# Performance work log

Hardware: AMD Instinct MI355X
Metric: run time of the kernel (lower is better)

## Reference

```python
import jax, jax.numpy as jnp
import numpy as np

EMBED = 1024
HEADS = 16
HEAD_DIM = EMBED // HEADS
BATCH = 8
SEQ = 2048


def setup_inputs() -> dict:
    key = jax.random.key(0)
    ks = jax.random.split(key, 6)
    s = EMBED ** -0.5
    x = jax.random.normal(ks[0], (BATCH, SEQ, EMBED), dtype=jnp.float32)
    # weights stored as (in, out); applied as x @ W (equivalent to torch Linear with W.T)
    Wq = jax.random.normal(ks[1], (EMBED, EMBED), dtype=jnp.float32) * s
    Wk = jax.random.normal(ks[2], (EMBED, EMBED), dtype=jnp.float32) * s
    Wv = jax.random.normal(ks[3], (EMBED, EMBED), dtype=jnp.float32) * s
    Wo = jax.random.normal(ks[4], (EMBED, EMBED), dtype=jnp.float32) * s
    bo = jax.random.normal(ks[5], (EMBED,), dtype=jnp.float32) * 0.01
    return {"x": x, "Wq": Wq, "Wk": Wk, "Wv": Wv, "Wo": Wo, "bo": bo}


def reference(x, Wq, Wk, Wv, Wo, bo):
    N, S, E = x.shape
    H, D = HEADS, HEAD_DIM
    # project and reshape to (N, H, S, D) exactly as the torch code (view + permute)
    q = (x @ Wq).reshape(N, S, H, D).transpose(0, 2, 1, 3)
    k = (x @ Wk).reshape(N, S, H, D).transpose(0, 2, 1, 3)
    v = (x @ Wv).reshape(N, S, H, D).transpose(0, 2, 1, 3)
    # Faithful to source: einsum subscripts applied to ALREADY-PERMUTED tensors,
    # so 'a'/'b' range over heads and 's' over seq -> energy is (N, H, H).
    energy = jnp.einsum('nasd,nbsd->nab', q, k)
    attention = jax.nn.softmax(energy / np.sqrt(D).astype(np.float32), axis=2)
    # second einsum: sum over key-heads (b) and value-heads (h) independently
    out = jnp.einsum('nab,nhsd->nasd', attention, v)  # (N, H, S, D)
    out = out.transpose(0, 2, 1, 3).reshape(N, S, E)
    return out @ Wo + bo
```

## Files before the change

kernel.cpp:

```cpp
#include <hip/hip_runtime.h>
#include <hip/hip_bf16.h>


typedef __attribute__((ext_vector_type(8))) short bf16x8;
typedef __attribute__((ext_vector_type(4))) float f32x4;

__device__ __forceinline__ unsigned short f2bf(float f) {
  unsigned int u = __builtin_bit_cast(unsigned int, f);
  u += 0x7FFFu + ((u >> 16) & 1u);
  return (unsigned short)(u >> 16);
}
__device__ __forceinline__ float bf2f(unsigned short b) {
  unsigned int u = ((unsigned int)b) << 16;
  return __builtin_bit_cast(float, u);
}
__device__ __forceinline__ unsigned int pack2(unsigned short a, unsigned short b) {
  return (unsigned int)a | ((unsigned int)b << 16);
}
__device__ __forceinline__ void split2(float a, float b, unsigned int& hi, unsigned int& lo) {
  unsigned short ha = f2bf(a), hb = f2bf(b);
  hi = pack2(ha, hb);
  lo = pack2(f2bf(a - bf2f(ha)), f2bf(b - bf2f(hb)));
}
__device__ __forceinline__ bf16x8 asbf(uint4 u) { return __builtin_bit_cast(bf16x8, u); }

__global__ __launch_bounds__(256) void prep(const float* __restrict__ Wv,
                                            const float* __restrict__ Wo,
                                            unsigned short* __restrict__ BvF,
                                            unsigned short* __restrict__ BoF) {
  const int b = blockIdx.x, t = threadIdx.x;
  const int l = t & 63, lr = l & 15, lk = (l >> 4) << 3;
  if (b < 32) {
    const int s = b, ctg = t >> 6;
    const int d = (ctg << 4) + lr;
    const int k0 = (s << 5) + lk;
    float sum[8] = {};
#pragma unroll
    for (int h = 0; h < 16; ++h)
#pragma unroll
      for (int j = 0; j < 8; ++j)
        sum[j] += Wv[(k0 + j) * 1024 + h * 64 + d];
    unsigned short hh[8], ll[8];
#pragma unroll
    for (int j = 0; j < 8; ++j) {
      hh[j] = f2bf(sum[j]);
      ll[j] = f2bf(sum[j] - bf2f(hh[j]));
    }
    const int base = ((s * 4 + ctg) * 2) * 64 + l;
    uint4 uh = make_uint4(pack2(hh[0], hh[1]), pack2(hh[2], hh[3]),
                          pack2(hh[4], hh[5]), pack2(hh[6], hh[7]));
    uint4 ul = make_uint4(pack2(ll[0], ll[1]), pack2(ll[2], ll[3]),
                          pack2(ll[4], ll[5]), pack2(ll[6], ll[7]));
    ((uint4*)BvF)[base] = uh;
    ((uint4*)BvF)[base + 64] = ul;
  } else {
    const int ctg2 = b - 32;
    const int kk = t >> 7, jh = (t >> 6) & 1;
    const int e = (ctg2 << 4) + lr;
    const int kb = (kk << 5) + lk + (jh << 2);
    float sum[4] = {};
#pragma unroll
    for (int h = 0; h < 16; ++h)
#pragma unroll
      for (int j = 0; j < 4; ++j)
        sum[j] += Wo[(h * 64 + kb + j) * 1024 + e];
    unsigned short hh[4], ll[4];
#pragma unroll
    for (int j = 0; j < 4; ++j) {
      hh[j] = f2bf(sum[j]);
      ll[j] = f2bf(sum[j] - bf2f(hh[j]));
    }
    const int base = ((((ctg2 * 2 + kk) * 2) * 64 + l) << 1) + jh;
    ((uint2*)BoF)[base] = make_uint2(pack2(hh[0], hh[1]), pack2(hh[2], hh[3]));
    ((uint2*)BoF)[base + 128] = make_uint2(pack2(ll[0], ll[1]), pack2(ll[2], ll[3]));
  }
}

__global__ __launch_bounds__(256) void gemm1(const float* __restrict__ x,
                                             const unsigned short* __restrict__ BvF,
                                             unsigned short* __restrict__ tmph,
                                             unsigned short* __restrict__ tmpl) {
  __shared__ unsigned short Ah[2][32][72], Al[2][32][72];
  const int t = threadIdx.x;
  const int r0 = blockIdx.x << 5;
  const int w = t >> 6, l = t & 63;
  const int wr = (w >> 1) << 4;
  const int ctgb = (w & 1) << 1;
  const int lr = l & 15, lk = (l >> 4) << 3;
  const int srow = t >> 3, skg = (t & 7) << 3;
  const float* xp = &x[(r0 + srow) * 1024 + skg];
  const uint4* bp = (const uint4*)BvF;

  float4 xr[2][2];
  uint4 br[2][8];
  f32x4 acc[2] = {};

  xr[0][0] = *(const float4*)(xp);
  xr[0][1] = *(const float4*)(xp + 4);
  xr[1][0] = *(const float4*)(xp + 64);
  xr[1][1] = *(const float4*)(xp + 68);
#pragma unroll
  for (int kk = 0; kk < 2; ++kk)
#pragma unroll
    for (int ct = 0; ct < 2; ++ct)
#pragma unroll
      for (int hl = 0; hl < 2; ++hl)
        br[0][(kk * 2 + ct) * 2 + hl] =
            bp[((kk * 4 + ctgb + ct) * 2 + hl) * 64 + l];
  {
    unsigned int h0, h1, h2, h3, q0, q1, q2, q3;
    split2(xr[0][0].x, xr[0][0].y, h0, q0);
    split2(xr[0][0].z, xr[0][0].w, h1, q1);
    split2(xr[0][1].x, xr[0][1].y, h2, q2);
    split2(xr[0][1].z, xr[0][1].w, h3, q3);
    *(uint4*)&Ah[0][srow][skg] = make_uint4(h0, h1, h2, h3);
    *(uint4*)&Al[0][srow][skg] = make_uint4(q0, q1, q2, q3);
  }

#pragma unroll
  for (int c = 0; c < 16; ++c) {
    const int buf = c & 1;
    if (c + 2 < 16) {
      const float* xq = xp + (c + 2) * 64;
      xr[buf][0] = *(const float4*)(xq);
      xr[buf][1] = *(const float4*)(xq + 4);
    }
    if (c + 1 < 16) {
#pragma unroll
      for (int kk = 0; kk < 2; ++kk)
#pragma unroll
        for (int ct = 0; ct < 2; ++ct)
#pragma unroll
          for (int hl = 0; hl < 2; ++hl)
            br[buf ^ 1][(kk * 2 + ct) * 2 + hl] =
                bp[((((c + 1) * 2 + kk) * 4 + ctgb + ct) * 2 + hl) * 64 + l];
    }
    __syncthreads();
#pragma unroll
    for (int kk = 0; kk < 2; ++kk) {
      bf16x8 ah = *(const bf16x8*)&Ah[buf][wr + lr][kk * 32 + lk];
      bf16x8 al = *(const bf16x8*)&Al[buf][wr + lr][kk * 32 + lk];
#pragma unroll
      for (int ct = 0; ct < 2; ++ct) {
        bf16x8 bh = asbf(br[buf][(kk * 2 + ct) * 2 + 0]);
        bf16x8 bl = asbf(br[buf][(kk * 2 + ct) * 2 + 1]);
        acc[ct] = __builtin_amdgcn_mfma_f32_16x16x32_bf16(ah, bh, acc[ct], 0, 0, 0);
        acc[ct] = __builtin_amdgcn_mfma_f32_16x16x32_bf16(ah, bl, acc[ct], 0, 0, 0);
        acc[ct] = __builtin_amdgcn_mfma_f32_16x16x32_bf16(al, bh, acc[ct], 0, 0, 0);
      }
    }
    if (c + 1 < 16) {
      unsigned int h0, h1, h2, h3, q0, q1, q2, q3;
      float4 a0 = xr[buf ^ 1][0], a1 = xr[buf ^ 1][1];
      split2(a0.x, a0.y, h0, q0);
      split2(a0.z, a0.w, h1, q1);
      split2(a1.x, a1.y, h2, q2);
      split2(a1.z, a1.w, h3, q3);
      *(uint4*)&Ah[buf ^ 1][srow][skg] = make_uint4(h0, h1, h2, h3);
      *(uint4*)&Al[buf ^ 1][srow][skg] = make_uint4(q0, q1, q2, q3);
    }
  }

  __syncthreads();
  {
    unsigned short* sh = &Ah[0][0][0];
    unsigned short* sl = &Al[0][0][0];
#pragma unroll
    for (int ct = 0; ct < 2; ++ct) {
      const int col = ((ctgb + ct) << 4) + lr;
#pragma unroll
      for (int j = 0; j < 4; ++j) {
        const int r = wr + ((l >> 4) << 2) + j;
        float v = acc[ct][j];
        unsigned short h = f2bf(v);
        sh[r * 72 + col] = h;
        sl[r * 72 + col] = f2bf(v - bf2f(h));
      }
    }
  }
  __syncthreads();
  {
    const int row = t >> 3, kg = (t & 7) << 3;
    uint4 vh = *(const uint4*)&Ah[0][row][kg];
    uint4 vl = *(const uint4*)&Al[0][row][kg];
    *(uint4*)&tmph[(r0 + row) * 64 + kg] = vh;
    *(uint4*)&tmpl[(r0 + row) * 64 + kg] = vl;
  }
}

__global__ __launch_bounds__(256) void gemm2(const unsigned short* __restrict__ tmph,
                                             const unsigned short* __restrict__ tmpl,
                                             const unsigned short* __restrict__ BoF,
                                             const float* __restrict__ bo,
                                             float* __restrict__ out) {
  __shared__ unsigned short Ah[64][72], Al[64][72];
  const int t = threadIdx.x;
  const int mb = blockIdx.x >> 1, nb = blockIdx.x & 1;
  const int r0 = mb << 6, c0 = nb << 9;
  const int l = t & 63, lr = l & 15, lk = (l >> 4) << 3;
  const int wr = (t >> 6) << 4;
  const uint4* bp = (const uint4*)BoF;

  {
    const int row = t >> 2, kg = (t & 3) << 4;
    const uint4* ph = (const uint4*)&tmph[(r0 + row) * 64 + kg];
    uint4 a0 = ph[0], a1 = ph[1];
    const uint4* pl4 = (const uint4*)&tmpl[(r0 + row) * 64 + kg];
    uint4 b0 = pl4[0], b1 = pl4[1];
    *(uint4*)&Ah[row][kg] = a0;
    *(uint4*)&Ah[row][kg + 8] = a1;
    *(uint4*)&Al[row][kg] = b0;
    *(uint4*)&Al[row][kg + 8] = b1;
  }
  uint4 brg[2][4];
  float bvr[2];
#pragma unroll
  for (int kk = 0; kk < 2; ++kk)
#pragma unroll
    for (int hl = 0; hl < 2; ++hl)
      brg[0][kk * 2 + hl] = bp[(((nb * 32) * 2 + kk) * 2 + hl) * 64 + l];
  bvr[0] = bo[c0 + lr];
  __syncthreads();

  bf16x8 afh[2], afl[2];
#pragma unroll
  for (int kk = 0; kk < 2; ++kk) {
    afh[kk] = *(const bf16x8*)&Ah[wr + lr][kk * 32 + lk];
    afl[kk] = *(const bf16x8*)&Al[wr + lr][kk * 32 + lk];
  }

#pragma unroll
  for (int ct = 0; ct < 32; ++ct) {
    if (ct + 1 < 32) {
#pragma unroll
      for (int kk = 0; kk < 2; ++kk)
#pragma unroll
        for (int hl = 0; hl < 2; ++hl)
          brg[(ct + 1) & 1][kk * 2 + hl] =
              bp[(((nb * 32 + ct + 1) * 2 + kk) * 2 + hl) * 64 + l];
      bvr[(ct + 1) & 1] = bo[c0 + ((ct + 1) << 4) + lr];
    }
    f32x4 a = {};
#pragma unroll
    for (int kk = 0; kk < 2; ++kk) {
      bf16x8 bh = asbf(brg[ct & 1][kk * 2 + 0]);
      bf16x8 bl = asbf(brg[ct & 1][kk * 2 + 1]);
      a = __builtin_amdgcn_mfma_f32_16x16x32_bf16(afh[kk], bh, a, 0, 0, 0);
      a = __builtin_amdgcn_mfma_f32_16x16x32_bf16(afh[kk], bl, a, 0, 0, 0);
      a = __builtin_amdgcn_mfma_f32_16x16x32_bf16(afl[kk], bh, a, 0, 0, 0);
    }
    const int col = c0 + (ct << 4) + lr;
    const float bv = bvr[ct & 1];
#pragma unroll
    for (int j = 0; j < 4; ++j)
      out[(r0 + wr + ((l >> 4) << 2) + j) * 1024 + col] = a[j] + bv;
  }
}

extern "C" void kernel_launch(void* const* d_in, const int* in_sizes, int n_in,
                              void* d_out, int out_size, void* d_ws, size_t ws_size,
                              hipStream_t stream) {
  const float* x = (const float*)d_in[0];
  const float* Wv = (const float*)d_in[3];
  const float* Wo = (const float*)d_in[4];
  const float* bo = (const float*)d_in[5];
  float* out = (float*)d_out;

  unsigned short* BvF = (unsigned short*)d_ws;
  unsigned short* BoF = BvF + 131072;
  unsigned short* tmph = BoF + 131072;
  unsigned short* tmpl = tmph + 1048576;

  prep<<<96, 256, 0, stream>>>(Wv, Wo, BvF, BoF);
  gemm1<<<512, 256, 0, stream>>>(x, BvF, tmph, tmpl);
  gemm2<<<512, 256, 0, stream>>>(tmph, tmpl, BoF, bo, out);
}
```

Baseline: 152.7 us.

## Fuse both GEMMs into one kernel with split-K reduction through shared memory

```diff
diff --git a/kernel.cpp b/kernel.cpp
--- a/kernel.cpp
+++ b/kernel.cpp
@@ -47,16 +47,14 @@
       ll[j] = f2bf(sum[j] - bf2f(hh[j]));
     }
     const int base = ((s * 4 + ctg) * 2) * 64 + l;
-    uint4 uh = make_uint4(pack2(hh[0], hh[1]), pack2(hh[2], hh[3]),
-                          pack2(hh[4], hh[5]), pack2(hh[6], hh[7]));
-    uint4 ul = make_uint4(pack2(ll[0], ll[1]), pack2(ll[2], ll[3]),
-                          pack2(ll[4], ll[5]), pack2(ll[6], ll[7]));
-    ((uint4*)BvF)[base] = uh;
-    ((uint4*)BvF)[base + 64] = ul;
+    ((uint4*)BvF)[base] = make_uint4(pack2(hh[0], hh[1]), pack2(hh[2], hh[3]),
+                                     pack2(hh[4], hh[5]), pack2(hh[6], hh[7]));
+    ((uint4*)BvF)[base + 64] = make_uint4(pack2(ll[0], ll[1]), pack2(ll[2], ll[3]),
+                                          pack2(ll[4], ll[5]), pack2(ll[6], ll[7]));
   } else {
-    const int ctg2 = b - 32;
+    const int g = b - 32;
     const int kk = t >> 7, jh = (t >> 6) & 1;
-    const int e = (ctg2 << 4) + lr;
+    const int e = (g << 4) + lr;
     const int kb = (kk << 5) + lk + (jh << 2);
     float sum[4] = {};
 #pragma unroll
@@ -70,190 +68,136 @@
       hh[j] = f2bf(sum[j]);
       ll[j] = f2bf(sum[j] - bf2f(hh[j]));
     }
-    const int base = ((((ctg2 * 2 + kk) * 2) * 64 + l) << 1) + jh;
+    const int base = ((((g * 2 + kk) * 2) * 64 + l) << 1) + jh;
     ((uint2*)BoF)[base] = make_uint2(pack2(hh[0], hh[1]), pack2(hh[2], hh[3]));
     ((uint2*)BoF)[base + 128] = make_uint2(pack2(ll[0], ll[1]), pack2(ll[2], ll[3]));
   }
 }
 
-__global__ __launch_bounds__(256) void gemm1(const float* __restrict__ x,
-                                             const unsigned short* __restrict__ BvF,
-                                             unsigned short* __restrict__ tmph,
-                                             unsigned short* __restrict__ tmpl) {
-  __shared__ unsigned short Ah[2][32][72], Al[2][32][72];
-  const int t = threadIdx.x;
-  const int r0 = blockIdx.x << 5;
-  const int w = t >> 6, l = t & 63;
-  const int wr = (w >> 1) << 4;
-  const int ctgb = (w & 1) << 1;
-  const int lr = l & 15, lk = (l >> 4) << 3;
-  const int srow = t >> 3, skg = (t & 7) << 3;
-  const float* xp = &x[(r0 + srow) * 1024 + skg];
-  const uint4* bp = (const uint4*)BvF;
-
-  float4 xr[2][2];
-  uint4 br[2][8];
-  f32x4 acc[2] = {};
-
-  xr[0][0] = *(const float4*)(xp);
-  xr[0][1] = *(const float4*)(xp + 4);
-  xr[1][0] = *(const float4*)(xp + 64);
-  xr[1][1] = *(const float4*)(xp + 68);
-#pragma unroll
-  for (int kk = 0; kk < 2; ++kk)
-#pragma unroll
-    for (int ct = 0; ct < 2; ++ct)
+__global__ __launch_bounds__(512, 4) void fused(const float* __restrict__ x,
+                                                const unsigned short* __restrict__ BvF,
+                                                const unsigned short* __restrict__ BoF,
+                                                const float* __restrict__ bo,
+                                                float* __restrict__ out) {
+  __shared__ float red[2][4][16][64];
+  __shared__ unsigned short Ah[2][16][72], Al[2][16][72];
+  const int t = threadIdx.x, w = t >> 6, l = t & 63;
+  const int rh = w >> 2, q = w & 3;
+  const int lr = l & 15, lk8 = (l >> 4) << 3;
+  const int r0 = (int)blockIdx.x << 5;
+  const int rb = r0 + (rh << 4);
+
+  {
+    const float* xp = &x[(rb + lr) * 1024 + (q << 8) + lk8];
+    const uint4* bp = (const uint4*)BvF;
+    f32x4 acc[4] = {};
+    float4 xv[2][2];
+    uint4 br[2][8];
+    xv[0][0] = *(const float4*)(xp);
+    xv[0][1] = *(const float4*)(xp + 4);
+#pragma unroll
+    for (int ct = 0; ct < 4; ++ct)
 #pragma unroll
       for (int hl = 0; hl < 2; ++hl)
-        br[0][(kk * 2 + ct) * 2 + hl] =
-            bp[((kk * 4 + ctgb + ct) * 2 + hl) * 64 + l];
-  {
-    unsigned int h0, h1, h2, h3, q0, q1, q2, q3;
-    split2(xr[0][0].x, xr[0][0].y, h0, q0);
-    split2(xr[0][0].z, xr[0][0].w, h1, q1);
-    split2(xr[0][1].x, xr[0][1].y, h2, q2);
-    split2(xr[0][1].z, xr[0][1].w, h3, q3);
-    *(uint4*)&Ah[0][srow][skg] = make_uint4(h0, h1, h2, h3);
-    *(uint4*)&Al[0][srow][skg] = make_uint4(q0, q1, q2, q3);
-  }
-
-#pragma unroll
-  for (int c = 0; c < 16; ++c) {
-    const int buf = c & 1;
-    if (c + 2 < 16) {
-      const float* xq = xp + (c + 2) * 64;
-      xr[buf][0] = *(const float4*)(xq);
-      xr[buf][1] = *(const float4*)(xq + 4);
-    }
-    if (c + 1 < 16) {
-#pragma unroll
-      for (int kk = 0; kk < 2; ++kk)
-#pragma unroll
-        for (int ct = 0; ct < 2; ++ct)
+        br[0][ct * 2 + hl] = bp[(((q * 8) * 4 + ct) * 2 + hl) * 64 + l];
+#pragma unroll
+    for (int kc = 0; kc < 8; ++kc) {
+      const int cur = kc & 1;
+      if (kc + 1 < 8) {
+        const float* xq = xp + (kc + 1) * 32;
+        xv[cur ^ 1][0] = *(const float4*)(xq);
+        xv[cur ^ 1][1] = *(const float4*)(xq + 4);
+#pragma unroll
+        for (int ct = 0; ct < 4; ++ct)
 #pragma unroll
           for (int hl = 0; hl < 2; ++hl)
-            br[buf ^ 1][(kk * 2 + ct) * 2 + hl] =
-                bp[((((c + 1) * 2 + kk) * 4 + ctgb + ct) * 2 + hl) * 64 + l];
-    }
-    __syncthreads();
-#pragma unroll
-    for (int kk = 0; kk < 2; ++kk) {
-      bf16x8 ah = *(const bf16x8*)&Ah[buf][wr + lr][kk * 32 + lk];
-      bf16x8 al = *(const bf16x8*)&Al[buf][wr + lr][kk * 32 + lk];
-#pragma unroll
-      for (int ct = 0; ct < 2; ++ct) {
-        bf16x8 bh = asbf(br[buf][(kk * 2 + ct) * 2 + 0]);
-        bf16x8 bl = asbf(br[buf][(kk * 2 + ct) * 2 + 1]);
+            br[cur ^ 1][ct * 2 + hl] =
+                bp[(((q * 8 + kc + 1) * 4 + ct) * 2 + hl) * 64 + l];
+      }
+      unsigned int h0, h1, h2, h3, q0, q1, q2, q3;
+      split2(xv[cur][0].x, xv[cur][0].y, h0, q0);
+      split2(xv[cur][0].z, xv[cur][0].w, h1, q1);
+      split2(xv[cur][1].x, xv[cur][1].y, h2, q2);
+      split2(xv[cur][1].z, xv[cur][1].w, h3, q3);
+      bf16x8 ah = asbf(make_uint4(h0, h1, h2, h3));
+      bf16x8 al = asbf(make_uint4(q0, q1, q2, q3));
+#pragma unroll
+      for (int ct = 0; ct < 4; ++ct) {
+        bf16x8 bh = asbf(br[cur][ct * 2 + 0]);
+        bf16x8 bl = asbf(br[cur][ct * 2 + 1]);
         acc[ct] = __builtin_amdgcn_mfma_f32_16x16x32_bf16(ah, bh, acc[ct], 0, 0, 0);
         acc[ct] = __builtin_amdgcn_mfma_f32_16x16x32_bf16(ah, bl, acc[ct], 0, 0, 0);
         acc[ct] = __builtin_amdgcn_mfma_f32_16x16x32_bf16(al, bh, acc[ct], 0, 0, 0);
       }
     }
-    if (c + 1 < 16) {
-      unsigned int h0, h1, h2, h3, q0, q1, q2, q3;
-      float4 a0 = xr[buf ^ 1][0], a1 = xr[buf ^ 1][1];
-      split2(a0.x, a0.y, h0, q0);
-      split2(a0.z, a0.w, h1, q1);
-      split2(a1.x, a1.y, h2, q2);
-      split2(a1.z, a1.w, h3, q3);
-      *(uint4*)&Ah[buf ^ 1][srow][skg] = make_uint4(h0, h1, h2, h3);
-      *(uint4*)&Al[buf ^ 1][srow][skg] = make_uint4(q0, q1, q2, q3);
-    }
-  }
-
+#pragma unroll
+    for (int ct = 0; ct < 4; ++ct)
+#pragma unroll
+      for (int j = 0; j < 4; ++j)
+        red[rh][q][((l >> 4) << 2) + j][(ct << 4) + lr] = acc[ct][j];
+  }
   __syncthreads();
   {
-    unsigned short* sh = &Ah[0][0][0];
-    unsigned short* sl = &Al[0][0][0];
-#pragma unroll
-    for (int ct = 0; ct < 2; ++ct) {
-      const int col = ((ctgb + ct) << 4) + lr;
-#pragma unroll
-      for (int j = 0; j < 4; ++j) {
-        const int r = wr + ((l >> 4) << 2) + j;
-        float v = acc[ct][j];
-        unsigned short h = f2bf(v);
-        sh[r * 72 + col] = h;
-        sl[r * 72 + col] = f2bf(v - bf2f(h));
-      }
-    }
+    const int rh2 = t >> 8, row = (t >> 4) & 15, c4 = (t & 15) << 2;
+    float4 s = *(const float4*)&red[rh2][0][row][c4];
+    const float4 s1 = *(const float4*)&red[rh2][1][row][c4];
+    const float4 s2 = *(const float4*)&red[rh2][2][row][c4];
+    const float4 s3 = *(const float4*)&red[rh2][3][row][c4];
+    s.x += s1.x + s2.x + s3.x;
+    s.y += s1.y + s2.y + s3.y;
+    s.z += s1.z + s2.z + s3.z;
+    s.w += s1.w + s2.w + s3.w;
+    unsigned int h01, l01, h23, l23;
+    split2(s.x, s.y, h01, l01);
+    split2(s.z, s.w, h23, l23);
+    *(uint2*)&Ah[rh2][row][c4] = make_uint2(h01, h23);
+    *(uint2*)&Al[rh2][row][c4] = make_uint2(l01, l23);
   }
   __syncthreads();
   {
-    const int row = t >> 3, kg = (t & 7) << 3;
-    uint4 vh = *(const uint4*)&Ah[0][row][kg];
-    uint4 vl = *(const uint4*)&Al[0][row][kg];
-    *(uint4*)&tmph[(r0 + row) * 64 + kg] = vh;
-    *(uint4*)&tmpl[(r0 + row) * 64 + kg] = vl;
-  }
-}
-
-__global__ __launch_bounds__(256) void gemm2(const unsigned short* __restrict__ tmph,
-                                             const unsigned short* __restrict__ tmpl,
-                                             const unsigned short* __restrict__ BoF,
-                                             const float* __restrict__ bo,
-                                             float* __restrict__ out) {
-  __shared__ unsigned short Ah[64][72], Al[64][72];
-  const int t = threadIdx.x;
-  const int mb = blockIdx.x >> 1, nb = blockIdx.x & 1;
-  const int r0 = mb << 6, c0 = nb << 9;
-  const int l = t & 63, lr = l & 15, lk = (l >> 4) << 3;
-  const int wr = (t >> 6) << 4;
-  const uint4* bp = (const uint4*)BoF;
-
-  {
-    const int row = t >> 2, kg = (t & 3) << 4;
-    const uint4* ph = (const uint4*)&tmph[(r0 + row) * 64 + kg];
-    uint4 a0 = ph[0], a1 = ph[1];
-    const uint4* pl4 = (const uint4*)&tmpl[(r0 + row) * 64 + kg];
-    uint4 b0 = pl4[0], b1 = pl4[1];
-    *(uint4*)&Ah[row][kg] = a0;
-    *(uint4*)&Ah[row][kg + 8] = a1;
-    *(uint4*)&Al[row][kg] = b0;
-    *(uint4*)&Al[row][kg + 8] = b1;
-  }
-  uint4 brg[2][4];
-  float bvr[2];
-#pragma unroll
-  for (int kk = 0; kk < 2; ++kk)
-#pragma unroll
-    for (int hl = 0; hl < 2; ++hl)
-      brg[0][kk * 2 + hl] = bp[(((nb * 32) * 2 + kk) * 2 + hl) * 64 + l];
-  bvr[0] = bo[c0 + lr];
-  __syncthreads();
-
-  bf16x8 afh[2], afl[2];
-#pragma unroll
-  for (int kk = 0; kk < 2; ++kk) {
-    afh[kk] = *(const bf16x8*)&Ah[wr + lr][kk * 32 + lk];
-    afl[kk] = *(const bf16x8*)&Al[wr + lr][kk * 32 + lk];
-  }
-
-#pragma unroll
-  for (int ct = 0; ct < 32; ++ct) {
-    if (ct + 1 < 32) {
-#pragma unroll
-      for (int kk = 0; kk < 2; ++kk)
-#pragma unroll
-        for (int hl = 0; hl < 2; ++hl)
-          brg[(ct + 1) & 1][kk * 2 + hl] =
-              bp[(((nb * 32 + ct + 1) * 2 + kk) * 2 + hl) * 64 + l];
-      bvr[(ct + 1) & 1] = bo[c0 + ((ct + 1) << 4) + lr];
-    }
-    f32x4 a = {};
+    bf16x8 afh[2], afl[2];
 #pragma unroll
     for (int kk = 0; kk < 2; ++kk) {
-      bf16x8 bh = asbf(brg[ct & 1][kk * 2 + 0]);
-      bf16x8 bl = asbf(brg[ct & 1][kk * 2 + 1]);
-      a = __builtin_amdgcn_mfma_f32_16x16x32_bf16(afh[kk], bh, a, 0, 0, 0);
-      a = __builtin_amdgcn_mfma_f32_16x16x32_bf16(afh[kk], bl, a, 0, 0, 0);
-      a = __builtin_amdgcn_mfma_f32_16x16x32_bf16(afl[kk], bh, a, 0, 0, 0);
-    }
-    const int col = c0 + (ct << 4) + lr;
-    const float bv = bvr[ct & 1];
-#pragma unroll
-    for (int j = 0; j < 4; ++j)
-      out[(r0 + wr + ((l >> 4) << 2) + j) * 1024 + col] = a[j] + bv;
+      afh[kk] = *(const bf16x8*)&Ah[rh][lr][kk * 32 + lk8];
+      afl[kk] = *(const bf16x8*)&Al[rh][lr][kk * 32 + lk8];
+    }
+    const uint4* bp = (const uint4*)BoF;
+    uint4 brg[2][4];
+    float bvr[2];
+    const int g0 = q << 4;
+#pragma unroll
+    for (int kk = 0; kk < 2; ++kk)
+#pragma unroll
+      for (int hl = 0; hl < 2; ++hl)
+        brg[0][kk * 2 + hl] = bp[((g0 * 2 + kk) * 2 + hl) * 64 + l];
+    bvr[0] = bo[(g0 << 4) + lr];
+#pragma unroll
+    for (int ct = 0; ct < 16; ++ct) {
+      const int cur = ct & 1;
+      if (ct + 1 < 16) {
+        const int g = g0 + ct + 1;
+#pragma unroll
+        for (int kk = 0; kk < 2; ++kk)
+#pragma unroll
+          for (int hl = 0; hl < 2; ++hl)
+            brg[cur ^ 1][kk * 2 + hl] = bp[((g * 2 + kk) * 2 + hl) * 64 + l];
+        bvr[cur ^ 1] = bo[(g << 4) + lr];
+      }
+      f32x4 a = {};
+#pragma unroll
+      for (int kk = 0; kk < 2; ++kk) {
+        bf16x8 bh = asbf(brg[cur][kk * 2 + 0]);
+        bf16x8 bl = asbf(brg[cur][kk * 2 + 1]);
+        a = __builtin_amdgcn_mfma_f32_16x16x32_bf16(afh[kk], bh, a, 0, 0, 0);
+        a = __builtin_amdgcn_mfma_f32_16x16x32_bf16(afh[kk], bl, a, 0, 0, 0);
+        a = __builtin_amdgcn_mfma_f32_16x16x32_bf16(afl[kk], bh, a, 0, 0, 0);
+      }
+      const int col = (q << 8) + (ct << 4) + lr;
+      const float bv = bvr[cur];
+#pragma unroll
+      for (int j = 0; j < 4; ++j)
+        out[(rb + ((l >> 4) << 2) + j) * 1024 + col] = a[j] + bv;
+    }
   }
 }
 
@@ -268,10 +212,7 @@
 
   unsigned short* BvF = (unsigned short*)d_ws;
   unsigned short* BoF = BvF + 131072;
-  unsigned short* tmph = BoF + 131072;
-  unsigned short* tmpl = tmph + 1048576;
 
   prep<<<96, 256, 0, stream>>>(Wv, Wo, BvF, BoF);
-  gemm1<<<512, 256, 0, stream>>>(x, BvF, tmph, tmpl);
-  gemm2<<<512, 256, 0, stream>>>(tmph, tmpl, BoF, bo, out);
-}
+  fused<<<512, 512, 0, stream>>>(x, BvF, BoF, bo, out);
+}
```

Result: slower. 159.8 us (+4.7%).
